# Kernel optimization log

Measured on AMD Instinct MI355X. Metric: run time of the kernel, lower is better.

The kernel has to match this reference:

```python
import jax, jax.numpy as jnp
import numpy as np

B, L, D = 4, 2048, 1024
E, K, H = 8, 2, 4096      # num_experts, top_k, expert hidden (mlp_ratio=4)
HS = 4096                 # shared expert hidden (n_shared_experts=1 * 4*D)
EPS = 1e-6


def setup_inputs() -> dict:
    key = jax.random.key(0)
    ks = jax.random.split(key, 12)
    s = 0.02
    return {
        "x": jax.random.normal(ks[0], (B, L, D), jnp.float32),
        "time_c": jax.random.normal(ks[1], (B, D), jnp.float32),
        # AdaptiveLayerNorm: cond -> (shift, scale)
        "ada_w": jax.random.normal(ks[2], (D, 2 * D), jnp.float32) * s,
        "ada_b": jnp.zeros((2 * D,), jnp.float32),
        # router gate
        "gate_w": jax.random.normal(ks[3], (D, E), jnp.float32) * s,
        # routed experts (stacked)
        "w1": jax.random.normal(ks[4], (E, D, H), jnp.float32) * s,
        "b1": jnp.zeros((E, H), jnp.float32),
        "w2": jax.random.normal(ks[5], (E, H, D), jnp.float32) * s,
        "b2": jnp.zeros((E, D), jnp.float32),
        # shared expert
        "sw1": jax.random.normal(ks[6], (D, HS), jnp.float32) * s,
        "sb1": jnp.zeros((HS,), jnp.float32),
        "sw2": jax.random.normal(ks[7], (HS, D), jnp.float32) * s,
        "sb2": jnp.zeros((D,), jnp.float32),
    }


def _forward(x, time_c, ada_w, ada_b, gate_w, w1, b1, w2, b2, sw1, sb1, sw2, sb2):
    # --- AdaptiveLayerNorm: LN (no affine) modulated by time condition ---
    mu = jnp.mean(x, axis=-1, keepdims=True)
    var = jnp.var(x, axis=-1, keepdims=True)
    ln = (x - mu) * jax.lax.rsqrt(var + EPS)                       # (B,L,D)
    cond = jax.nn.silu(time_c) @ ada_w + ada_b                     # (B,2D)
    shift, scale = jnp.split(cond, 2, axis=-1)                     # (B,D) each
    xn = ln * (1.0 + scale[:, None, :]) + shift[:, None, :]        # (B,L,D)

    # --- SparseMoeBlock ---
    t = xn.reshape(B * L, D)                                       # (T,D) tokens
    probs = jax.nn.softmax(t @ gate_w, axis=-1)                    # (T,E)
    topv, topi = jax.lax.top_k(probs, K)                           # (T,K)
    topv = topv / jnp.sum(topv, axis=-1, keepdims=True)            # renormalize
    # dense per-expert combine weights via one-hot scatter: (T,E)
    w_dense = jnp.sum(jax.nn.one_hot(topi, E, dtype=t.dtype) * topv[..., None], axis=1)

    # shared expert applied to every token
    y = jax.nn.gelu(t @ sw1 + sb1) @ sw2 + sb2                     # (T,D)
    # routed experts: weighted combine (loop over fixed small E)
    for e in range(E):
        h = jax.nn.gelu(t @ w1[e] + b1[e])                         # (T,H)
        y = y + w_dense[:, e:e + 1] * (h @ w2[e] + b2[e])

    return x + y.reshape(B, L, D)                                  # residual


def reference(x, time_c, ada_w, ada_b, gate_w, w1, b1, w2, b2, sw1, sb1, sw2, sb2):
    return _forward(x, time_c, ada_w, ada_b, gate_w, w1, b1, w2, b2, sw1, sb1, sw2, sb2)
```

## Files before the change

kernel.cpp:

```cpp
#include <hip/hip_runtime.h>
#include <hip/hip_bf16.h>
#include <cstdint>

#define T_TOKENS 8192
#define DMODEL   1024
#define DHID     4096
#define NEXP     8

typedef float  f32x4  __attribute__((ext_vector_type(4)));
typedef __bf16 bf16x8 __attribute__((ext_vector_type(8)));

__device__ __forceinline__ void async_copy16(const void* gp, void* lp) {
    __builtin_amdgcn_global_load_lds(
        (const __attribute__((address_space(1))) void*)gp,
        (__attribute__((address_space(3))) void*)lp, 16, 0, 0);
}

__device__ __forceinline__ float gelu_tanh(float x) {
    float u = 0.7978845608028654f * (x + 0.044715f * x * x * x);
    return 0.5f * x * (1.0f + tanhf(u));
}

__global__ void transpose_cvt(const float* __restrict__ src,
                              __hip_bfloat16* __restrict__ dst, int R, int C) {
    __shared__ float tile[32][33];
    int bz = blockIdx.z;
    const float* s = src + (size_t)bz * R * C;
    __hip_bfloat16* d = dst + (size_t)bz * R * C;
    int c0 = blockIdx.x * 32, r0 = blockIdx.y * 32;
    int tx = threadIdx.x, ty = threadIdx.y;
#pragma unroll
    for (int i = 0; i < 4; i++) {
        int r = r0 + ty + i * 8;
        tile[ty + i * 8][tx] = s[(size_t)r * C + c0 + tx];
    }
    __syncthreads();
#pragma unroll
    for (int i = 0; i < 4; i++) {
        int c = c0 + ty + i * 8;
        d[(size_t)c * R + r0 + tx] = __float2bfloat16(tile[tx][ty + i * 8]);
    }
}

__global__ void cond_kernel(const float* __restrict__ time_c,
                            const float* __restrict__ ada_w,
                            const float* __restrict__ ada_b,
                            float* __restrict__ cond) {
    __shared__ float sl[DMODEL];
    int b = blockIdx.x >> 3;
    int j = ((blockIdx.x & 7) << 8) + threadIdx.x;
    for (int i = threadIdx.x; i < DMODEL; i += 256) {
        float tc = time_c[b * DMODEL + i];
        sl[i] = tc / (1.0f + __expf(-tc));
    }
    __syncthreads();
    float acc = ada_b[j];
    for (int i = 0; i < DMODEL; i++)
        acc += sl[i] * ada_w[(size_t)i * 2048 + j];
    cond[b * 2048 + j] = acc;
}

__global__ __launch_bounds__(256) void ln_gate_kernel(
    const float* __restrict__ x, const float* __restrict__ cond,
    const float* __restrict__ gate_w,
    __hip_bfloat16* __restrict__ xnb,
    int* __restrict__ topi, float* __restrict__ topw, int* __restrict__ counts) {
    int t = blockIdx.x;
    int b = t >> 11;
    int tid = threadIdx.x, lane = tid & 63, wave = tid >> 6;
    const float4* xr = (const float4*)(x + (size_t)t * DMODEL);
    float4 v = xr[tid];
    float s = v.x + v.y + v.z + v.w;
    float q = v.x * v.x + v.y * v.y + v.z * v.z + v.w * v.w;
#pragma unroll
    for (int o = 32; o > 0; o >>= 1) {
        s += __shfl_down(s, o, 64);
        q += __shfl_down(q, o, 64);
    }
    __shared__ float red[8];
    if (lane == 0) { red[wave] = s; red[4 + wave] = q; }
    __syncthreads();
    float tsum = red[0] + red[1] + red[2] + red[3];
    float tsq  = red[4] + red[5] + red[6] + red[7];
    float mu   = tsum * (1.0f / DMODEL);
    float var  = tsq * (1.0f / DMODEL) - mu * mu;
    float rstd = rsqrtf(var + 1e-6f);

    int j = tid * 4;
    const float4* cb = (const float4*)(cond + (size_t)b * 2048);
    float4 sh = cb[tid];
    float4 sc = cb[256 + tid];
    float xv[4];
    xv[0] = (v.x - mu) * rstd * (1.0f + sc.x) + sh.x;
    xv[1] = (v.y - mu) * rstd * (1.0f + sc.y) + sh.y;
    xv[2] = (v.z - mu) * rstd * (1.0f + sc.z) + sh.z;
    xv[3] = (v.w - mu) * rstd * (1.0f + sc.w) + sh.w;
    union { ushort4 u4; __hip_bfloat16 h[4]; } pk;
#pragma unroll
    for (int r = 0; r < 4; r++) pk.h[r] = __float2bfloat16(xv[r]);
    *((ushort4*)(xnb + (size_t)t * DMODEL + j)) = pk.u4;

    float g[8] = {0, 0, 0, 0, 0, 0, 0, 0};
    const float4* gw = (const float4*)gate_w;
#pragma unroll
    for (int r = 0; r < 4; r++) {
        float4 ga = gw[(j + r) * 2];
        float4 gb = gw[(j + r) * 2 + 1];
        g[0] += xv[r] * ga.x; g[1] += xv[r] * ga.y;
        g[2] += xv[r] * ga.z; g[3] += xv[r] * ga.w;
        g[4] += xv[r] * gb.x; g[5] += xv[r] * gb.y;
        g[6] += xv[r] * gb.z; g[7] += xv[r] * gb.w;
    }
#pragma unroll
    for (int e = 0; e < 8; e++) {
#pragma unroll
        for (int o = 32; o > 0; o >>= 1) g[e] += __shfl_down(g[e], o, 64);
    }
    __shared__ float gred[4][8];
    if (lane == 0) {
#pragma unroll
        for (int e = 0; e < 8; e++) gred[wave][e] = g[e];
    }
    __syncthreads();
    if (tid == 0) {
        float l[8];
#pragma unroll
        for (int e = 0; e < 8; e++)
            l[e] = gred[0][e] + gred[1][e] + gred[2][e] + gred[3][e];
        int i0 = 0; float v0 = l[0];
        int i1 = -1; float v1 = -3.4e38f;
        for (int e = 1; e < 8; e++) {
            if (l[e] > v0) { v1 = v0; i1 = i0; v0 = l[e]; i0 = e; }
            else if (l[e] > v1) { v1 = l[e]; i1 = e; }
        }
        float r = __expf(v1 - v0);
        float w0 = 1.0f / (1.0f + r);
        topi[2 * t] = i0; topi[2 * t + 1] = i1;
        topw[2 * t] = w0; topw[2 * t + 1] = 1.0f - w0;
        atomicAdd(&counts[i0], 1);
        atomicAdd(&counts[i1], 1);
    }
}

__global__ void scan_kernel(const int* __restrict__ counts,
                            int* __restrict__ offs, int* __restrict__ cursors) {
    if (threadIdx.x == 0) {
        int a = 0;
        for (int e = 0; e < NEXP; e++) { offs[e] = a; cursors[e] = a; a += counts[e]; }
    }
}

__global__ void fill_kernel(const int* __restrict__ topi, const float* __restrict__ topw,
                            int* __restrict__ cursors,
                            int* __restrict__ rowlist, float* __restrict__ wlist) {
    int t = blockIdx.x * 256 + threadIdx.x;
#pragma unroll
    for (int k = 0; k < 2; k++) {
        int e = topi[2 * t + k];
        int pos = atomicAdd(&cursors[e], 1);
        rowlist[pos] = t;
        wlist[pos] = topw[2 * t + k];
    }
}

template <int MODE>
__global__ __launch_bounds__(256, 4) void gemm_bt(
    const __hip_bfloat16* __restrict__ A,
    const __hip_bfloat16* __restrict__ Bt,
    const float* __restrict__ bias,
    const float* __restrict__ xres,
    float* __restrict__ outf,
    __hip_bfloat16* __restrict__ outb,
    const int* __restrict__ rowlist,
    const float* __restrict__ wlist,
    const int* __restrict__ offs,
    const int* __restrict__ counts,
    int K, int N) {
    int e = 0, seg_off = 0, Mcnt = 0;
    if constexpr (MODE >= 2) {
        e = blockIdx.z;
        Mcnt = counts[e];
        if ((int)blockIdx.x * 128 >= Mcnt) return;
        seg_off = offs[e];
    }
    const __hip_bfloat16* Bte = Bt + (size_t)e * (size_t)N * K;
    const float* biase = bias + (size_t)e * N;
    int row0 = blockIdx.x * 128, col0 = blockIdx.y * 128;

    __shared__ __align__(16) __hip_bfloat16 sA[128 * 64];
    __shared__ __align__(16) __hip_bfloat16 sB[128 * 64];

    int tid = threadIdx.x, wave = tid >> 6, lane = tid & 63;
    int wm = wave >> 1, wn = wave & 1;

    int kc = ((lane & 7) ^ (lane >> 3)) * 8;
    const __hip_bfloat16* aptr[4];
    const __hip_bfloat16* bptr[4];
#pragma unroll
    for (int i = 0; i < 4; i++) {
        int c = wave * 4 + i;
        int rr = c * 8 + (lane >> 3);
        size_t arow;
        if constexpr (MODE == 0 || MODE == 1) {
            arow = (size_t)(row0 + rr);
        } else {
            int p = row0 + rr; if (p > Mcnt - 1) p = Mcnt - 1;
            arow = (MODE == 2) ? (size_t)rowlist[seg_off + p] : (size_t)(seg_off + p);
        }
        aptr[i] = A + arow * K + kc;
        int nn = col0 + c * 8 + (lane >> 3);
        bptr[i] = Bte + (size_t)nn * K + kc;
    }

    f32x4 acc[4][4];
#pragma unroll
    for (int tm = 0; tm < 4; tm++)
#pragma unroll
        for (int tn = 0; tn < 4; tn++) acc[tm][tn] = (f32x4){0.f, 0.f, 0.f, 0.f};

    char* sAc = (char*)&sA[0];
    char* sBc = (char*)&sB[0];

    for (int k0 = 0; k0 < K; k0 += 64) {
#pragma unroll
        for (int i = 0; i < 4; i++) {
            int c = wave * 4 + i;
            async_copy16(aptr[i], sAc + c * 1024);
            async_copy16(bptr[i], sBc + c * 1024);
            aptr[i] += 64;
            bptr[i] += 64;
        }
        asm volatile("s_waitcnt vmcnt(0)" ::: "memory");
        __syncthreads();
        const short* sa = (const short*)sAc;
        const short* sb = (const short*)sBc;
#pragma unroll
        for (int kk = 0; kk < 64; kk += 32) {
            int kbc = (kk >> 3) + (lane >> 4);
            int swz = ((kbc ^ (lane & 7)) << 3);
            bf16x8 af[4], bfr[4];
#pragma unroll
            for (int tm = 0; tm < 4; tm++)
                af[tm] = *(const bf16x8*)(sa + (size_t)(wm * 64 + tm * 16 + (lane & 15)) * 64 + swz);
#pragma unroll
            for (int tn = 0; tn < 4; tn++)
                bfr[tn] = *(const bf16x8*)(sb + (size_t)(wn * 64 + tn * 16 + (lane & 15)) * 64 + swz);
#pragma unroll
            for (int tm = 0; tm < 4; tm++)
#pragma unroll
                for (int tn = 0; tn < 4; tn++)
                    acc[tm][tn] = __builtin_amdgcn_mfma_f32_16x16x32_bf16(
                        af[tm], bfr[tn], acc[tm][tn], 0, 0, 0);
        }
        __syncthreads();
    }

#pragma unroll
    for (int tm = 0; tm < 4; tm++) {
#pragma unroll
        for (int tn = 0; tn < 4; tn++) {
            int c = col0 + wn * 64 + tn * 16 + (lane & 15);
            int rbase = wm * 64 + tm * 16 + ((lane >> 4) << 2);
            float bb = biase[c];
#pragma unroll
            for (int i = 0; i < 4; i++) {
                int rl = rbase + i;
                float v = acc[tm][tn][i] + bb;
                if constexpr (MODE == 0) {
                    outb[(size_t)(row0 + rl) * N + c] = __float2bfloat16(gelu_tanh(v));
                } else if constexpr (MODE == 1) {
                    size_t idx = (size_t)(row0 + rl) * N + c;
                    outf[idx] = xres[idx] + v;
                } else if constexpr (MODE == 2) {
                    int p = row0 + rl;
                    if (p < Mcnt)
                        outb[(size_t)(seg_off + p) * N + c] = __float2bfloat16(gelu_tanh(v));
                } else {
                    int p = row0 + rl;
                    if (p < Mcnt) {
                        int tok = rowlist[seg_off + p];
                        float w = wlist[seg_off + p];
                        atomicAdd(&outf[(size_t)tok * N + c], w * v);
                    }
                }
            }
        }
    }
}

extern "C" void kernel_launch(void* const* d_in, const int* in_sizes, int n_in,
                              void* d_out, int out_size, void* d_ws, size_t ws_size,
                              hipStream_t stream) {
    const float* x      = (const float*)d_in[0];
    const float* time_c = (const float*)d_in[1];
    const float* ada_w  = (const float*)d_in[2];
    const float* ada_b  = (const float*)d_in[3];
    const float* gate_w = (const float*)d_in[4];
    const float* w1     = (const float*)d_in[5];
    const float* b1     = (const float*)d_in[6];
    const float* w2     = (const float*)d_in[7];
    const float* b2     = (const float*)d_in[8];
    const float* sw1    = (const float*)d_in[9];
    const float* sb1    = (const float*)d_in[10];
    const float* sw2    = (const float*)d_in[11];
    const float* sb2    = (const float*)d_in[12];
    float* out = (float*)d_out;
    (void)in_sizes; (void)n_in; (void)out_size; (void)ws_size;

    char* ws = (char*)d_ws;
    size_t off = 0;
    auto alloc = [&](size_t bytes) -> char* {
        char* p = ws + off;
        off += (bytes + 255) & ~(size_t)255;
        return p;
    };
    __hip_bfloat16* xnb  = (__hip_bfloat16*)alloc((size_t)T_TOKENS * DMODEL * 2);
    __hip_bfloat16* w1t  = (__hip_bfloat16*)alloc((size_t)NEXP * DMODEL * DHID * 2);
    __hip_bfloat16* w2t  = (__hip_bfloat16*)alloc((size_t)NEXP * DMODEL * DHID * 2);
    __hip_bfloat16* sw1t = (__hip_bfloat16*)alloc((size_t)DMODEL * DHID * 2);
    __hip_bfloat16* sw2t = (__hip_bfloat16*)alloc((size_t)DMODEL * DHID * 2);
    __hip_bfloat16* hs   = (__hip_bfloat16*)alloc((size_t)T_TOKENS * DHID * 2);
    __hip_bfloat16* hr   = (__hip_bfloat16*)alloc((size_t)2 * T_TOKENS * DHID * 2);
    float* cond    = (float*)alloc(4 * 2048 * 4);
    int*   topi    = (int*)alloc(T_TOKENS * 2 * 4);
    float* topw    = (float*)alloc(T_TOKENS * 2 * 4);
    int*   rowlist = (int*)alloc(2 * T_TOKENS * 4);
    float* wlist   = (float*)alloc(2 * T_TOKENS * 4);
    int*   counts  = (int*)alloc(256);
    int*   offs    = (int*)alloc(256);
    int*   cursors = (int*)alloc(256);

    hipMemsetAsync(counts, 0, NEXP * sizeof(int), stream);

    dim3 tb(32, 8);
    transpose_cvt<<<dim3(128, 32, 8), tb, 0, stream>>>(w1, w1t, 1024, 4096);
    transpose_cvt<<<dim3(32, 128, 8), tb, 0, stream>>>(w2, w2t, 4096, 1024);
    transpose_cvt<<<dim3(128, 32, 1), tb, 0, stream>>>(sw1, sw1t, 1024, 4096);
    transpose_cvt<<<dim3(32, 128, 1), tb, 0, stream>>>(sw2, sw2t, 4096, 1024);

    cond_kernel<<<32, 256, 0, stream>>>(time_c, ada_w, ada_b, cond);
    ln_gate_kernel<<<T_TOKENS, 256, 0, stream>>>(x, cond, gate_w, xnb, topi, topw, counts);
    scan_kernel<<<1, 64, 0, stream>>>(counts, offs, cursors);
    fill_kernel<<<32, 256, 0, stream>>>(topi, topw, cursors, rowlist, wlist);

    gemm_bt<0><<<dim3(64, 32), 256, 0, stream>>>(xnb, sw1t, sb1, nullptr, nullptr, hs,
                                                 nullptr, nullptr, nullptr, nullptr, 1024, 4096);
    gemm_bt<1><<<dim3(64, 8), 256, 0, stream>>>(hs, sw2t, sb2, x, out, nullptr,
                                                nullptr, nullptr, nullptr, nullptr, 4096, 1024);
    gemm_bt<2><<<dim3(64, 32, 8), 256, 0, stream>>>(xnb, w1t, b1, nullptr, nullptr, hr,
                                                    rowlist, nullptr, offs, counts, 1024, 4096);
    gemm_bt<3><<<dim3(64, 8, 8), 256, 0, stream>>>(hr, w2t, b2, nullptr, out, nullptr,
                                                   rowlist, wlist, offs, counts, 4096, 1024);
}
```

Baseline: 1.540 ms.

## Replace atomic scatter in expert down-projection with dense store plus combine kernel

The routed-expert second GEMM now writes weighted outputs densely into a permuted scratch buffer, reusing the shared hidden buffer, instead of doing per-element atomicAdds to scattered token rows. The fill kernel records each token's slot positions, and a new combine kernel gathers the two expert outputs per token and adds them to the residual output. This is meant to remove the cost of contended, uncoalesced float atomics. In exchange it adds an extra kernel launch and an extra round trip of about 64 MB of fp32 scratch writes and reads.

```diff
diff --git a/kernel.cpp b/kernel.cpp
--- a/kernel.cpp
+++ b/kernel.cpp
@@ -152,7 +152,8 @@
 
 __global__ void fill_kernel(const int* __restrict__ topi, const float* __restrict__ topw,
                             int* __restrict__ cursors,
-                            int* __restrict__ rowlist, float* __restrict__ wlist) {
+                            int* __restrict__ rowlist, float* __restrict__ wlist,
+                            int* __restrict__ slots) {
     int t = blockIdx.x * 256 + threadIdx.x;
 #pragma unroll
     for (int k = 0; k < 2; k++) {
@@ -160,7 +161,25 @@
         int pos = atomicAdd(&cursors[e], 1);
         rowlist[pos] = t;
         wlist[pos] = topw[2 * t + k];
-    }
+        slots[2 * t + k] = pos;
+    }
+}
+
+__global__ __launch_bounds__(256) void combine_kernel(
+    const int* __restrict__ slots, const float* __restrict__ yr,
+    float* __restrict__ out) {
+    int t = blockIdx.x;
+    int p0 = slots[2 * t], p1 = slots[2 * t + 1];
+    int i = threadIdx.x;
+    const float4* a = (const float4*)(yr + (size_t)p0 * DMODEL);
+    const float4* b = (const float4*)(yr + (size_t)p1 * DMODEL);
+    float4* o = (float4*)(out + (size_t)t * DMODEL);
+    float4 va = a[i], vb = b[i], vo = o[i];
+    vo.x += va.x + vb.x;
+    vo.y += va.y + vb.y;
+    vo.z += va.z + vb.z;
+    vo.w += va.w + vb.w;
+    o[i] = vo;
 }
 
 template <int MODE>
@@ -257,10 +276,18 @@
 
 #pragma unroll
     for (int tm = 0; tm < 4; tm++) {
+        int rbase = wm * 64 + tm * 16 + ((lane >> 4) << 2);
+        float wv[4];
+        if constexpr (MODE == 3) {
+#pragma unroll
+            for (int i = 0; i < 4; i++) {
+                int p = row0 + rbase + i;
+                wv[i] = (p < Mcnt) ? wlist[seg_off + p] : 0.0f;
+            }
+        }
 #pragma unroll
         for (int tn = 0; tn < 4; tn++) {
             int c = col0 + wn * 64 + tn * 16 + (lane & 15);
-            int rbase = wm * 64 + tm * 16 + ((lane >> 4) << 2);
             float bb = biase[c];
 #pragma unroll
             for (int i = 0; i < 4; i++) {
@@ -277,11 +304,8 @@
                         outb[(size_t)(seg_off + p) * N + c] = __float2bfloat16(gelu_tanh(v));
                 } else {
                     int p = row0 + rl;
-                    if (p < Mcnt) {
-                        int tok = rowlist[seg_off + p];
-                        float w = wlist[seg_off + p];
-                        atomicAdd(&outf[(size_t)tok * N + c], w * v);
-                    }
+                    if (p < Mcnt)
+                        outf[(size_t)(seg_off + p) * N + c] = wv[i] * v;
                 }
             }
         }
@@ -326,9 +350,11 @@
     float* topw    = (float*)alloc(T_TOKENS * 2 * 4);
     int*   rowlist = (int*)alloc(2 * T_TOKENS * 4);
     float* wlist   = (float*)alloc(2 * T_TOKENS * 4);
+    int*   slots   = (int*)alloc(2 * T_TOKENS * 4);
     int*   counts  = (int*)alloc(256);
     int*   offs    = (int*)alloc(256);
     int*   cursors = (int*)alloc(256);
+    float* yr = (float*)hs;
 
     hipMemsetAsync(counts, 0, NEXP * sizeof(int), stream);
 
@@ -341,7 +367,7 @@
     cond_kernel<<<32, 256, 0, stream>>>(time_c, ada_w, ada_b, cond);
     ln_gate_kernel<<<T_TOKENS, 256, 0, stream>>>(x, cond, gate_w, xnb, topi, topw, counts);
     scan_kernel<<<1, 64, 0, stream>>>(counts, offs, cursors);
-    fill_kernel<<<32, 256, 0, stream>>>(topi, topw, cursors, rowlist, wlist);
+    fill_kernel<<<32, 256, 0, stream>>>(topi, topw, cursors, rowlist, wlist, slots);
 
     gemm_bt<0><<<dim3(64, 32), 256, 0, stream>>>(xnb, sw1t, sb1, nullptr, nullptr, hs,
                                                  nullptr, nullptr, nullptr, nullptr, 1024, 4096);
@@ -349,6 +375,7 @@
                                                 nullptr, nullptr, nullptr, nullptr, 4096, 1024);
     gemm_bt<2><<<dim3(64, 32, 8), 256, 0, stream>>>(xnb, w1t, b1, nullptr, nullptr, hr,
                                                     rowlist, nullptr, offs, counts, 1024, 4096);
-    gemm_bt<3><<<dim3(64, 8, 8), 256, 0, stream>>>(hr, w2t, b2, nullptr, out, nullptr,
-                                                   rowlist, wlist, offs, counts, 4096, 1024);
-}
+    gemm_bt<3><<<dim3(64, 8, 8), 256, 0, stream>>>(hr, w2t, b2, nullptr, yr, nullptr,
+                                                   nullptr, wlist, offs, counts, 4096, 1024);
+    combine_kernel<<<T_TOKENS, 256, 0, stream>>>(slots, yr, out);
+}
```

New measurement: 1.523 ms. Within noise of the previous version (-1.2%).
